# Kernel tuning notes

Measured on AMD Instinct MI355X. Metric: run time of the kernel, lower is better.

## Reference

```python
import jax, jax.numpy as jnp
import numpy as np

B, C, H, W = 8, 64, 16, 16
TE = 128      # te_hidden
GT = 256      # rn_gt_hidden
FP = 256      # rn_fp_hidden
A = 32        # a_size
O = H * W
PAIR_IN = (C + 2) * 2 + TE  # 260, matches (cv_filter+2)*2 + te_hidden


def setup_inputs() -> dict:
    key = jax.random.key(0)
    ks = jax.random.split(key, 10)

    def w(k, fan_in, fan_out):
        return (jax.random.normal(k, (fan_in, fan_out), jnp.float32)
                / np.sqrt(fan_in).astype(np.float32))

    return {
        "x": jax.random.normal(ks[0], (B, C, H, W), jnp.float32),
        "code": jax.random.normal(ks[1], (B, TE), jnp.float32),
        "gt_w1": w(ks[2], PAIR_IN, GT), "gt_b1": jnp.zeros((GT,), jnp.float32),
        "gt_w2": w(ks[3], GT, GT),      "gt_b2": jnp.zeros((GT,), jnp.float32),
        "gt_w3": w(ks[4], GT, GT),      "gt_b3": jnp.zeros((GT,), jnp.float32),
        "fp_w1": w(ks[5], GT, FP),      "fp_b1": jnp.zeros((FP,), jnp.float32),
        "fp_w2": w(ks[6], FP, FP),      "fp_b2": jnp.zeros((FP,), jnp.float32),
        "fp_w3": w(ks[7], FP, A),       "fp_b3": jnp.zeros((A,), jnp.float32),
    }


def _coords(h, w):
    # 2 normalized coordinate channels in [-1, 1], one value per object
    ys = jnp.linspace(-1.0, 1.0, h, dtype=jnp.float32)
    xs = jnp.linspace(-1.0, 1.0, w, dtype=jnp.float32)
    yy, xx = jnp.meshgrid(ys, xs, indexing="ij")
    return jnp.stack([yy.ravel(), xx.ravel()], axis=-1)  # (o, 2)


def reference(x, code, gt_w1, gt_b1, gt_w2, gt_b2, gt_w3, gt_b3,
              fp_w1, fp_b1, fp_w2, fp_b2, fp_w3, fp_b3):
    b, c, h, w = x.shape
    o = h * w
    te = code.shape[-1]

    # rn_encode: flatten spatial grid to objects, append 2 coord channels
    xo = x.reshape(b, c, o).transpose(0, 2, 1)                 # (b, o, c)
    coord = jnp.broadcast_to(_coords(h, w)[None], (b, o, 2))
    xo = jnp.concatenate([xo, coord], axis=-1)                 # (b, o, c+2)

    # all O^2 ordered pairs + broadcast question code
    xi = jnp.broadcast_to(xo[:, :, None, :], (b, o, o, c + 2))
    xj = jnp.broadcast_to(xo[:, None, :, :], (b, o, o, c + 2))
    q = jnp.broadcast_to(code[:, None, None, :], (b, o, o, te))
    pairs = jnp.concatenate([xi, xj, q], axis=-1)              # (b, o, o, PAIR_IN)

    # g_theta MLP (ReLU after every layer)
    h1 = jax.nn.relu(pairs @ gt_w1 + gt_b1)
    h2 = jax.nn.relu(h1 @ gt_w2 + gt_b2)
    rel = jax.nn.relu(h2 @ gt_w3 + gt_b3)                      # (b, o, o, GT)

    # lower_sum: sum relations over the lower-triangular (i >= j) pairs
    mask = jnp.tril(jnp.ones((o, o), rel.dtype))
    summed = jnp.einsum("bijd,ij->bd", rel, mask)              # (b, GT)

    # f_phi MLP; no activation on final logits, dropout=0 (eval)
    f1 = jax.nn.relu(summed @ fp_w1 + fp_b1)
    f2 = jax.nn.relu(f1 @ fp_w2 + fp_b2)
    logits = f2 @ fp_w3 + fp_b3                                # (b, A)
    return logits
```

## Files before the change

kernel.cpp:

```cpp
#include <hip/hip_runtime.h>
#include <stdint.h>


#define NPAIR 32896
#define NPT   129

using short8  = __attribute__((ext_vector_type(8))) short;
using float4v = __attribute__((ext_vector_type(4))) float;

__device__ __forceinline__ float asf(unsigned u) {
    union { unsigned u; float f; } c; c.u = u; return c.f;
}
__device__ __forceinline__ unsigned short f2bf(float f) {
    union { float f; unsigned u; } c; c.f = f;
    unsigned u = c.u;
    u += 0x7FFFu + ((u >> 16) & 1u);
    return (unsigned short)(u >> 16);
}
__device__ __forceinline__ unsigned cvtpk(float lo, float hi) {
    unsigned r;
    asm("v_cvt_pk_bf16_f32 %0, %1, %2" : "=v"(r) : "v"(lo), "v"(hi));
    return r;
}
__device__ __forceinline__ void ij_of(int p, int& i, int& j) {
    float s = sqrtf(8.0f * (float)p + 1.0f);
    i = (int)((s - 1.0f) * 0.5f);
    while ((i + 1) * (i + 2) / 2 <= p) ++i;
    while (i * (i + 1) / 2 > p) --i;
    j = p - i * (i + 1) / 2;
}
__device__ __forceinline__ short8 buildA(uint4 uu, uint4 vv) {
    unsigned ua[4] = {uu.x, uu.y, uu.z, uu.w};
    unsigned va[4] = {vv.x, vv.y, vv.z, vv.w};
    union { unsigned u[4]; short8 s; } c;
    #pragma unroll
    for (int q = 0; q < 4; ++q) {
        float lo = asf(ua[q] << 16)         + asf(va[q] << 16);
        float hi = asf(ua[q] & 0xFFFF0000u) + asf(va[q] & 0xFFFF0000u);
        c.u[q] = cvtpk(fmaxf(lo, 0.f), fmaxf(hi, 0.f));
    }
    return c.s;
}

__global__ __launch_bounds__(256) void k_pre(
    const float* __restrict__ x, const float* __restrict__ code,
    const float* __restrict__ w1, const float* __restrict__ b1,
    const float* __restrict__ w2, const float* __restrict__ w3,
    unsigned short* __restrict__ ub, unsigned short* __restrict__ vb,
    unsigned short* __restrict__ w2t, unsigned short* __restrict__ w3t,
    float* __restrict__ summed)
{
    const int tid = threadIdx.x;
    if (blockIdx.x < 32) {
        const int ig = blockIdx.x, b = blockIdx.y, d = tid;
        float q = b1[d];
        const float* cp = code + b * 128;
        #pragma unroll 16
        for (int t = 0; t < 128; ++t) q += cp[t] * w1[(132 + t) * 256 + d];
        float su[8], sv[8];
        #pragma unroll
        for (int k = 0; k < 8; ++k) { su[k] = q; sv[k] = 0.f; }
        const float* xp = x + (b * 64) * 256 + ig * 8;
        #pragma unroll 8
        for (int c = 0; c < 64; ++c) {
            const float wu = w1[c * 256 + d];
            const float wv = w1[(66 + c) * 256 + d];
            const float* xc = xp + c * 256;
            #pragma unroll
            for (int k = 0; k < 8; ++k) { su[k] += xc[k] * wu; sv[k] += xc[k] * wv; }
        }
        const float wyu = w1[64 * 256 + d],  wxu = w1[65 * 256 + d];
        const float wyv = w1[130 * 256 + d], wxv = w1[131 * 256 + d];
        #pragma unroll
        for (int k = 0; k < 8; ++k) {
            const int i = ig * 8 + k;
            const float yy = (float)(i >> 4) * (2.0f / 15.0f) - 1.0f;
            const float xx = (float)(i & 15) * (2.0f / 15.0f) - 1.0f;
            ub[(b * 256 + i) * 256 + d] = f2bf(su[k] + yy * wyu + xx * wxu);
            vb[(b * 256 + i) * 256 + d] = f2bf(sv[k] + yy * wyv + xx * wxv);
        }
    } else {
        __shared__ float t[64][65];
        const int y = blockIdx.y;
        summed[y * 256 + tid] = 0.f;
        const int tx = tid & 63, ty = tid >> 6;
        for (int jj = 0; jj < 4; ++jj) {
            const int job = y * 4 + jj;
            const float* src = (job & 16) ? w3 : w2;
            unsigned short* dst = (job & 16) ? w3t : w2t;
            const int k0 = ((job >> 2) & 3) * 64, n0 = (job & 3) * 64;
            __syncthreads();
            #pragma unroll
            for (int r = ty; r < 64; r += 4) t[r][tx] = src[(k0 + r) * 256 + n0 + tx];
            __syncthreads();
            #pragma unroll
            for (int r = ty; r < 64; r += 4) dst[(n0 + r) * 256 + k0 + tx] = f2bf(t[tx][r]);
        }
    }
}

__global__ __launch_bounds__(512) void k_fuse(
    const unsigned short* __restrict__ ub, const unsigned short* __restrict__ vb,
    const unsigned short* __restrict__ w2t, const unsigned short* __restrict__ w3t,
    const float* __restrict__ b2, const float* __restrict__ b3,
    float* __restrict__ summed)
{
    extern __shared__ unsigned short lds[];
    const int tid  = threadIdx.x;
    const int pt   = blockIdx.x, b = blockIdx.y;
    const int lane = tid & 63, w = tid >> 6;
    const int lm   = lane & 15, quad = lane >> 4;

    #pragma unroll
    for (int it = 0; it < 16; ++it) {
        const int idx = it * 512 + tid;
        const int n = idx >> 5, c = idx & 31;
        const uint4 d = *(const uint4*)(w2t + n * 256 + c * 8);
        *(uint4*)(&lds[n * 256 + ((c ^ (n & 7)) << 3)]) = d;
    }

    const unsigned short* up[2];
    const unsigned short* vp[2];
    #pragma unroll
    for (int mt = 0; mt < 2; ++mt) {
        const int p0 = pt * 256 + w * 32 + mt * 16 + lm;
        const int p  = p0 < NPAIR ? p0 : NPAIR - 1;
        int i, j; ij_of(p, i, j);
        up[mt] = ub + ((b * 256 + i) * 256) + quad * 8;
        vp[mt] = vb + ((b * 256 + j) * 256) + quad * 8;
    }
    const int wave_valid = (pt * 256 + w * 32) < NPAIR;
    __syncthreads();

    const float4v zero4 = {0.f, 0.f, 0.f, 0.f};

    float4v acc1[2][16];
    #pragma unroll
    for (int mt = 0; mt < 2; ++mt)
        #pragma unroll
        for (int nt = 0; nt < 16; ++nt) acc1[mt][nt] = zero4;
    {
        uint4 cu[2][2], cv[2][2];
        #pragma unroll
        for (int kk = 0; kk < 2; ++kk)
            #pragma unroll
            for (int mt = 0; mt < 2; ++mt) {
                cu[kk][mt] = *(const uint4*)(up[mt] + kk * 32);
                cv[kk][mt] = *(const uint4*)(vp[mt] + kk * 32);
            }
        for (int ks = 0; ks < 8; ++ks) {
            const int pr = ks & 1;
            short8 afr[2];
            #pragma unroll
            for (int mt = 0; mt < 2; ++mt) afr[mt] = buildA(cu[pr][mt], cv[pr][mt]);
            if (ks < 6) {
                #pragma unroll
                for (int mt = 0; mt < 2; ++mt) {
                    cu[pr][mt] = *(const uint4*)(up[mt] + (ks + 2) * 32);
                    cv[pr][mt] = *(const uint4*)(vp[mt] + (ks + 2) * 32);
                }
            }
            const int coff = ((ks * 4 + quad) ^ (lm & 7)) << 3;
            __builtin_amdgcn_s_setprio(1);
            #pragma unroll
            for (int ng = 0; ng < 4; ++ng) {
                short8 bfr[4];
                #pragma unroll
                for (int q = 0; q < 4; ++q)
                    bfr[q] = *(const short8*)(&lds[((ng * 4 + q) * 16 + lm) * 256 + coff]);
                #pragma unroll
                for (int mt = 0; mt < 2; ++mt)
                    #pragma unroll
                    for (int q = 0; q < 4; ++q)
                        acc1[mt][ng * 4 + q] = __builtin_amdgcn_mfma_f32_16x16x32_bf16(
                            afr[mt], bfr[q], acc1[mt][ng * 4 + q], 0, 0, 0);
            }
            __builtin_amdgcn_s_setprio(0);
        }
    }
    __syncthreads();

    const unsigned short* bb3 = w3t + ((w * 32 + lm) * 256) + quad * 8;
    short8 bbuf[2][2];
    #pragma unroll
    for (int kk = 0; kk < 2; ++kk)
        #pragma unroll
        for (int nt = 0; nt < 2; ++nt)
            bbuf[kk][nt] = *(const short8*)(bb3 + nt * 4096 + kk * 32);

    const float msk = wave_valid ? 1.f : 0.f;
    #pragma unroll
    for (int nt = 0; nt < 16; ++nt) {
        const float bb = b2[nt * 16 + lm];
        const int col = nt * 16 + lm;
        #pragma unroll
        for (int mt = 0; mt < 2; ++mt) {
            const int rbase = w * 32 + mt * 16 + quad * 4;
            const float v0 = fmaxf(acc1[mt][nt][0] + bb, 0.f) * msk;
            const float v1 = fmaxf(acc1[mt][nt][1] + bb, 0.f) * msk;
            const float v2 = fmaxf(acc1[mt][nt][2] + bb, 0.f) * msk;
            const float v3 = fmaxf(acc1[mt][nt][3] + bb, 0.f) * msk;
            const unsigned w01 = cvtpk(v0, v1), w23 = cvtpk(v2, v3);
            const int c0 = col >> 3, c7 = col & 7;
            lds[(rbase + 0) * 256 + (((c0 ^ ((rbase + 0) & 7)) << 3) | c7)] =
                (unsigned short)w01;
            lds[(rbase + 1) * 256 + (((c0 ^ ((rbase + 1) & 7)) << 3) | c7)] =
                (unsigned short)(w01 >> 16);
            lds[(rbase + 2) * 256 + (((c0 ^ ((rbase + 2) & 7)) << 3) | c7)] =
                (unsigned short)w23;
            lds[(rbase + 3) * 256 + (((c0 ^ ((rbase + 3) & 7)) << 3) | c7)] =
                (unsigned short)(w23 >> 16);
        }
    }
    __syncthreads();

    float4v acc2[16][2];
    #pragma unroll
    for (int mt = 0; mt < 16; ++mt)
        #pragma unroll
        for (int nt = 0; nt < 2; ++nt) acc2[mt][nt] = zero4;
    {
        for (int ks = 0; ks < 8; ++ks) {
            const int pr = ks & 1;
            short8 bcur[2];
            #pragma unroll
            for (int nt = 0; nt < 2; ++nt) bcur[nt] = bbuf[pr][nt];
            if (ks < 6) {
                #pragma unroll
                for (int nt = 0; nt < 2; ++nt)
                    bbuf[pr][nt] = *(const short8*)(bb3 + nt * 4096 + (ks + 2) * 32);
            }
            __builtin_amdgcn_s_setprio(1);
            #pragma unroll
            for (int mt = 0; mt < 16; ++mt) {
                const int row = mt * 16 + lm;
                const short8 a = *(const short8*)(
                    &lds[row * 256 + (((ks * 4 + quad) ^ (row & 7)) << 3)]);
                #pragma unroll
                for (int nt = 0; nt < 2; ++nt)
                    acc2[mt][nt] = __builtin_amdgcn_mfma_f32_16x16x32_bf16(
                        a, bcur[nt], acc2[mt][nt], 0, 0, 0);
            }
            __builtin_amdgcn_s_setprio(0);
        }
    }

    #pragma unroll
    for (int nt = 0; nt < 2; ++nt) {
        const int col = w * 32 + nt * 16 + lm;
        const float bb = b3[col];
        float s = 0.f;
        #pragma unroll
        for (int mt = 0; mt < 16; ++mt)
            #pragma unroll
            for (int rg = 0; rg < 4; ++rg)
                s += fmaxf(acc2[mt][nt][rg] + bb, 0.f);
        s += __shfl_xor(s, 16);
        s += __shfl_xor(s, 32);
        if (quad == 0)
            atomicAdd(&summed[b * 256 + col], s);
    }
}

__global__ __launch_bounds__(1024) void k_tail(
    const float* __restrict__ summed,
    const float* __restrict__ fw1, const float* __restrict__ fb1,
    const float* __restrict__ fw2, const float* __restrict__ fb2,
    const float* __restrict__ fw3, const float* __restrict__ fb3,
    float* __restrict__ out)
{
    __shared__ float s0[256], s1[256], red[1024];
    const int b = blockIdx.x, tid = threadIdx.x;
    const int d = tid & 255, kh = tid >> 8;
    if (tid < 256) s0[tid] = summed[b * 256 + tid];
    __syncthreads();
    float p = 0.f;
    #pragma unroll 16
    for (int k = kh * 64; k < kh * 64 + 64; ++k) p += s0[k] * fw1[k * 256 + d];
    red[kh * 256 + d] = p;
    __syncthreads();
    if (tid < 256)
        s1[tid] = fmaxf(red[tid] + red[256 + tid] + red[512 + tid] + red[768 + tid]
                        + fb1[tid], 0.f);
    __syncthreads();
    p = 0.f;
    #pragma unroll 16
    for (int k = kh * 64; k < kh * 64 + 64; ++k) p += s1[k] * fw2[k * 256 + d];
    red[kh * 256 + d] = p;
    __syncthreads();
    if (tid < 256)
        s0[tid] = fmaxf(red[tid] + red[256 + tid] + red[512 + tid] + red[768 + tid]
                        + fb2[tid], 0.f);
    __syncthreads();
    const int d3 = tid & 31, kh3 = tid >> 5;
    p = 0.f;
    #pragma unroll
    for (int k = kh3 * 8; k < kh3 * 8 + 8; ++k) p += s0[k] * fw3[k * 32 + d3];
    red[kh3 * 32 + d3] = p;
    __syncthreads();
    if (tid < 32) {
        float o = fb3[tid];
        #pragma unroll 8
        for (int r = 0; r < 32; ++r) o += red[r * 32 + tid];
        out[b * 32 + tid] = o;
    }
}

extern "C" void kernel_launch(void* const* d_in, const int* in_sizes, int n_in,
                              void* d_out, int out_size, void* d_ws, size_t ws_size,
                              hipStream_t stream) {
    const float* x    = (const float*)d_in[0];
    const float* code = (const float*)d_in[1];
    const float* gw1  = (const float*)d_in[2];
    const float* gb1  = (const float*)d_in[3];
    const float* gw2  = (const float*)d_in[4];
    const float* gb2  = (const float*)d_in[5];
    const float* gw3  = (const float*)d_in[6];
    const float* gb3  = (const float*)d_in[7];
    const float* fw1  = (const float*)d_in[8];
    const float* fb1  = (const float*)d_in[9];
    const float* fw2  = (const float*)d_in[10];
    const float* fb2  = (const float*)d_in[11];
    const float* fw3  = (const float*)d_in[12];
    const float* fb3  = (const float*)d_in[13];
    float* out = (float*)d_out;

    char* ws = (char*)d_ws;
    unsigned short* ub  = (unsigned short*)(ws);
    unsigned short* vb  = (unsigned short*)(ws + 1048576);
    unsigned short* w2t = (unsigned short*)(ws + 2097152);
    unsigned short* w3t = (unsigned short*)(ws + 2228224);
    float* summed = (float*)(ws + 2359296);

    hipLaunchKernelGGL(k_pre, dim3(33, 8), dim3(256), 0, stream,
                       x, code, gw1, gb1, gw2, gw3, ub, vb, w2t, w3t, summed);
    hipLaunchKernelGGL(k_fuse, dim3(NPT, 8), dim3(512), 131072, stream,
                       ub, vb, w2t, w3t, gb2, gb3, summed);
    hipLaunchKernelGGL(k_tail, dim3(8), dim3(1024), 0, stream,
                       summed, fw1, fb1, fw2, fb2, fw3, fb3, out);
}
```

Baseline: 190.9 us.

## Transpose layer-1 MFMA operands for packed LDS stores and deepen input prefetch

Swaps the A/B operands of the first-layer MFMA so each lane holds four consecutive output columns of one row rather than four rows of one column. The epilogue can then load the bias as a float4 and write the bf16 results to LDS as one 8-byte store instead of four 2-byte scattered stores. It also deepens the global prefetch of pair inputs from two to three stages and fully unrolls the k-loop. The extra prefetch stage and the unrolling raise register pressure on top of the large accumulator array, which may reduce occupancy or cause spills.

```diff
diff --git a/kernel.cpp b/kernel.cpp
--- a/kernel.cpp
+++ b/kernel.cpp
@@ -134,30 +134,31 @@
 
     const float4v zero4 = {0.f, 0.f, 0.f, 0.f};
 
-    float4v acc1[2][16];
-    #pragma unroll
-    for (int mt = 0; mt < 2; ++mt)
-        #pragma unroll
-        for (int nt = 0; nt < 16; ++nt) acc1[mt][nt] = zero4;
+    float4v acc1[16][2];
+    #pragma unroll
+    for (int nt = 0; nt < 16; ++nt)
+        #pragma unroll
+        for (int mt = 0; mt < 2; ++mt) acc1[nt][mt] = zero4;
     {
-        uint4 cu[2][2], cv[2][2];
-        #pragma unroll
-        for (int kk = 0; kk < 2; ++kk)
+        uint4 cu[3][2], cv[3][2];
+        #pragma unroll
+        for (int kk = 0; kk < 3; ++kk)
             #pragma unroll
             for (int mt = 0; mt < 2; ++mt) {
                 cu[kk][mt] = *(const uint4*)(up[mt] + kk * 32);
                 cv[kk][mt] = *(const uint4*)(vp[mt] + kk * 32);
             }
+        #pragma unroll
         for (int ks = 0; ks < 8; ++ks) {
-            const int pr = ks & 1;
+            const int pr = ks % 3;
             short8 afr[2];
             #pragma unroll
             for (int mt = 0; mt < 2; ++mt) afr[mt] = buildA(cu[pr][mt], cv[pr][mt]);
-            if (ks < 6) {
+            if (ks < 5) {
                 #pragma unroll
                 for (int mt = 0; mt < 2; ++mt) {
-                    cu[pr][mt] = *(const uint4*)(up[mt] + (ks + 2) * 32);
-                    cv[pr][mt] = *(const uint4*)(vp[mt] + (ks + 2) * 32);
+                    cu[pr][mt] = *(const uint4*)(up[mt] + (ks + 3) * 32);
+                    cv[pr][mt] = *(const uint4*)(vp[mt] + (ks + 3) * 32);
                 }
             }
             const int coff = ((ks * 4 + quad) ^ (lm & 7)) << 3;
@@ -169,11 +170,11 @@
                 for (int q = 0; q < 4; ++q)
                     bfr[q] = *(const short8*)(&lds[((ng * 4 + q) * 16 + lm) * 256 + coff]);
                 #pragma unroll
-                for (int mt = 0; mt < 2; ++mt)
+                for (int q = 0; q < 4; ++q)
                     #pragma unroll
-                    for (int q = 0; q < 4; ++q)
-                        acc1[mt][ng * 4 + q] = __builtin_amdgcn_mfma_f32_16x16x32_bf16(
-                            afr[mt], bfr[q], acc1[mt][ng * 4 + q], 0, 0, 0);
+                    for (int mt = 0; mt < 2; ++mt)
+                        acc1[ng * 4 + q][mt] = __builtin_amdgcn_mfma_f32_16x16x32_bf16(
+                            bfr[q], afr[mt], acc1[ng * 4 + q][mt], 0, 0, 0);
             }
             __builtin_amdgcn_s_setprio(0);
         }
@@ -191,25 +192,17 @@
     const float msk = wave_valid ? 1.f : 0.f;
     #pragma unroll
     for (int nt = 0; nt < 16; ++nt) {
-        const float bb = b2[nt * 16 + lm];
-        const int col = nt * 16 + lm;
+        const float4 bbv = *(const float4*)(b2 + nt * 16 + quad * 4);
         #pragma unroll
         for (int mt = 0; mt < 2; ++mt) {
-            const int rbase = w * 32 + mt * 16 + quad * 4;
-            const float v0 = fmaxf(acc1[mt][nt][0] + bb, 0.f) * msk;
-            const float v1 = fmaxf(acc1[mt][nt][1] + bb, 0.f) * msk;
-            const float v2 = fmaxf(acc1[mt][nt][2] + bb, 0.f) * msk;
-            const float v3 = fmaxf(acc1[mt][nt][3] + bb, 0.f) * msk;
-            const unsigned w01 = cvtpk(v0, v1), w23 = cvtpk(v2, v3);
-            const int c0 = col >> 3, c7 = col & 7;
-            lds[(rbase + 0) * 256 + (((c0 ^ ((rbase + 0) & 7)) << 3) | c7)] =
-                (unsigned short)w01;
-            lds[(rbase + 1) * 256 + (((c0 ^ ((rbase + 1) & 7)) << 3) | c7)] =
-                (unsigned short)(w01 >> 16);
-            lds[(rbase + 2) * 256 + (((c0 ^ ((rbase + 2) & 7)) << 3) | c7)] =
-                (unsigned short)w23;
-            lds[(rbase + 3) * 256 + (((c0 ^ ((rbase + 3) & 7)) << 3) | c7)] =
-                (unsigned short)(w23 >> 16);
+            const int row = w * 32 + mt * 16 + lm;
+            const float v0 = fmaxf(acc1[nt][mt][0] + bbv.x, 0.f) * msk;
+            const float v1 = fmaxf(acc1[nt][mt][1] + bbv.y, 0.f) * msk;
+            const float v2 = fmaxf(acc1[nt][mt][2] + bbv.z, 0.f) * msk;
+            const float v3 = fmaxf(acc1[nt][mt][3] + bbv.w, 0.f) * msk;
+            uint2 pk; pk.x = cvtpk(v0, v1); pk.y = cvtpk(v2, v3);
+            const int c0 = nt * 2 + (quad >> 1);
+            *(uint2*)(&lds[row * 256 + (((c0 ^ (row & 7)) << 3) | ((quad & 1) << 2))]) = pk;
         }
     }
     __syncthreads();
```

Result: no change. 192.2 us (+0.6%).
